# Optimization experiments

Measured on AMD Instinct MI355X. Metric: run time of the kernel, lower is better.

Reference implementation:

```python
import jax, jax.numpy as jnp
import numpy as np

B, S, D, H = 2, 2048, 512, 8
DK = D // H
NEG = -1.0e9


def _xavier(key, shape):
    fan_in, fan_out = shape[-1], shape[0]
    lim = np.sqrt(6.0 / (fan_in + fan_out))
    return jax.random.uniform(key, shape, jnp.float32, -lim, lim)


def _rope_freqs(seq, dim):
    # lucidrains RotaryEmbedding: inv_freq over even dims, each freq repeated twice
    inv_freq = 1.0 / (10000.0 ** (jnp.arange(0, dim, 2, dtype=jnp.float32) / dim))
    freqs = jnp.arange(seq, dtype=jnp.float32)[:, None] * inv_freq[None, :]  # (S, dim/2)
    return jnp.repeat(freqs, 2, axis=-1)  # (S, dim)


def _rotate_half(x):
    xr = x.reshape(*x.shape[:-1], -1, 2)
    x1, x2 = xr[..., 0], xr[..., 1]
    return jnp.stack([-x2, x1], axis=-1).reshape(x.shape)


def _shift_down(s):
    # pad_zero row at position 0, drop last-but-keep rows 1: (concat trick)
    return jnp.concatenate([jnp.zeros_like(s[:, :, :1, :]), s[:, :, 1:, :]], axis=2)


def setup_inputs() -> dict:
    key = jax.random.key(0)
    kq, kk, kv, kt, kwq, kwk, kwv, kwo, kg = jax.random.split(key, 9)
    inp = {
        "q": jax.random.normal(kq, (B, S, D), jnp.float32),
        "k": jax.random.normal(kk, (B, S, D), jnp.float32),
        "v": jax.random.normal(kv, (B, S, D), jnp.float32),
        "ltime": jax.random.uniform(kt, (B, S), jnp.float32),
        "mask": jnp.broadcast_to(jnp.triu(jnp.ones((S, S), bool), k=1)[None], (B, S, S)),
        "Wq": _xavier(kwq, (D, D)), "bq": jnp.zeros((D,), jnp.float32),
        "Wk": _xavier(kwk, (D, D)), "bk": jnp.zeros((D,), jnp.float32),
        "Wv": _xavier(kwv, (D, D)), "bv": jnp.zeros((D,), jnp.float32),
        "Wo": _xavier(kwo, (D, D)), "bo": jnp.zeros((D,), jnp.float32),
        "gammas": jax.random.uniform(kg, (H, S, 1), jnp.float32, -0.1, 0.1),
    }
    return inp


def reference(q, k, v, ltime, mask, Wq, bq, Wk, bk, Wv, bv, Wo, bo, gammas):
    del ltime  # used only in dead code (dist_seq) in the original module

    def proj(x, W, b):
        return (x @ W.T + b).reshape(B, S, H, DK).transpose(0, 2, 1, 3)  # (B,H,S,DK)

    qh, kh, vh = proj(q, Wq, bq), proj(k, Wk, bk), proj(v, Wv, bv)

    freqs = _rope_freqs(S, DK)[None, None]  # (1,1,S,DK)
    cos, sin = jnp.cos(freqs), jnp.sin(freqs)
    qh = qh * cos + _rotate_half(qh) * sin
    kh = kh * cos + _rotate_half(kh) * sin

    scores = jnp.einsum("bhid,bhjd->bhij", qh, kh) / np.sqrt(DK)
    m = mask[:, None]  # (B,1,S,S)

    # --- no_grad distance-decay block ---
    s_ = jax.nn.softmax(jnp.where(m, NEG, scores), axis=-1)
    s_ = _shift_down(s_)
    distcum = jnp.cumsum(s_, axis=-1)
    disttot = jnp.sum(s_, axis=-1, keepdims=True)
    idx = jnp.arange(S, dtype=jnp.float32)
    pos_eff = jnp.abs(idx[None, :] - idx[:, None])[None, None]  # (1,1,S,S)
    dist = jax.lax.stop_gradient(
        jnp.sqrt(jnp.maximum((disttot - distcum) * pos_eff, 0.0)))

    g = -jax.nn.softplus(gammas)[None]  # (1,H,S,1)
    total_effect = jnp.clip(jnp.exp(dist * g), 1e-5, 1e5)
    scores = total_effect * scores

    scores = jax.nn.softmax(jnp.where(m, NEG, scores), axis=-1)
    scores = _shift_down(scores)

    out = jnp.einsum("bhij,bhjd->bhid", scores, vh)  # (B,H,S,DK)
    out = out.transpose(0, 2, 1, 3).reshape(B, S, D)
    return out @ Wo.T + bo
```

## Files before the change

### kernel.cpp

```cpp
#include <hip/hip_runtime.h>
#include <math.h>

#define B_ 2
#define S_ 2048
#define D_ 512
#define H_ 8
#define DK_ 64

typedef __attribute__((ext_vector_type(8))) short bf16x8;
typedef __attribute__((ext_vector_type(4))) float f32x4;

#define MFMA16(A, Bv, C) __builtin_amdgcn_mfma_f32_16x16x32_bf16(A, Bv, C, 0, 0, 0)

__device__ inline unsigned short f2bf(float x) {
  unsigned u = __float_as_uint(x);
  unsigned r = (u + 0x7fffu + ((u >> 16) & 1u)) >> 16;
  return (unsigned short)r;
}
__device__ inline unsigned pack2(float a, float b) {
  return (unsigned)f2bf(a) | ((unsigned)f2bf(b) << 16);
}

__global__ void rope_table_k(float* cs) {
  int idx = blockIdx.x * blockDim.x + threadIdx.x;
  if (idx >= S_ * 32) return;
  int s = idx >> 5, i = idx & 31;
  float invf = powf(10000.0f, -(float)(2 * i) / 64.0f);
  float ang = (float)s * invf;
  double a = (double)ang;
  cs[idx * 2]     = (float)cos(a);
  cs[idx * 2 + 1] = (float)sin(a);
}

__global__ __launch_bounds__(256)
void cvt3_k(const float* __restrict__ a, const float* __restrict__ b,
            const float* __restrict__ c, unsigned short* __restrict__ dst) {
  size_t idx = ((size_t)blockIdx.x * 256 + threadIdx.x) * 4;
  const size_t per = (size_t)4096 * 512;
  const float* src; size_t r;
  if (idx < per)            { src = a; r = idx; }
  else if (idx < 2 * per)   { src = b; r = idx - per; }
  else                      { src = c; r = idx - 2 * per; }
  float4 x = *(const float4*)(src + r);
  ushort4 y = { f2bf(x.x), f2bf(x.y), f2bf(x.z), f2bf(x.w) };
  *(ushort4*)(dst + idx) = y;
}
__global__ __launch_bounds__(256)
void cvt4_k(const float* __restrict__ a, const float* __restrict__ b,
            const float* __restrict__ c, const float* __restrict__ d,
            unsigned short* __restrict__ dst) {
  size_t idx = ((size_t)blockIdx.x * 256 + threadIdx.x) * 4;
  const size_t per = (size_t)512 * 512;
  const float* src; size_t r;
  if (idx < per)            { src = a; r = idx; }
  else if (idx < 2 * per)   { src = b; r = idx - per; }
  else if (idx < 3 * per)   { src = c; r = idx - 2 * per; }
  else                      { src = d; r = idx - 3 * per; }
  float4 x = *(const float4*)(src + r);
  ushort4 y = { f2bf(x.x), f2bf(x.y), f2bf(x.z), f2bf(x.w) };
  *(ushort4*)(dst + idx) = y;
}

__global__ __launch_bounds__(256)
void gemm_bf(const unsigned short* __restrict__ A,
             const unsigned short* __restrict__ W,
             const float* __restrict__ bias, void* __restrict__ Cout,
             const float* __restrict__ cs, int mode) {
  const int bm = blockIdx.y * 64, bn = blockIdx.x * 64;
  const int tid = threadIdx.x, w = tid >> 6, lane = tid & 63;
  const int li = lane & 15, lg = lane >> 4;
  __shared__ __align__(16) unsigned short As[64 * 64];
  __shared__ __align__(16) unsigned short Ws[64 * 64];
  f32x4 acc[4] = {{0.f,0.f,0.f,0.f},{0.f,0.f,0.f,0.f},{0.f,0.f,0.f,0.f},{0.f,0.f,0.f,0.f}};

  const int Bo0 = tid * 16, Bo1 = tid * 16 + 4096;
  const int r0 = Bo0 >> 7, c0 = Bo0 & 127;
  const int r1 = Bo1 >> 7, c1 = Bo1 & 127;
  const int so0 = (r0 * 128 + (c0 ^ ((r0 & 7) << 4))) >> 1;
  const int so1 = (r1 * 128 + (c1 ^ ((r1 & 7) << 4))) >> 1;

  const char* Abase = (const char*)A;
  const char* Wbase = (const char*)W;
  uint4 ra0 = *(const uint4*)(Abase + (size_t)(bm + r0) * 1024 + c0);
  uint4 ra1 = *(const uint4*)(Abase + (size_t)(bm + r1) * 1024 + c1);
  uint4 rw0 = *(const uint4*)(Wbase + (size_t)(bn + r0) * 1024 + c0);
  uint4 rw1 = *(const uint4*)(Wbase + (size_t)(bn + r1) * 1024 + c1);

  for (int t = 0; t < 8; ++t) {
    __syncthreads();
    *(uint4*)&As[so0] = ra0; *(uint4*)&As[so1] = ra1;
    *(uint4*)&Ws[so0] = rw0; *(uint4*)&Ws[so1] = rw1;
    __syncthreads();
    if (t < 7) {
      int k0 = (t + 1) * 128;
      ra0 = *(const uint4*)(Abase + (size_t)(bm + r0) * 1024 + k0 + c0);
      ra1 = *(const uint4*)(Abase + (size_t)(bm + r1) * 1024 + k0 + c1);
      rw0 = *(const uint4*)(Wbase + (size_t)(bn + r0) * 1024 + k0 + c0);
      rw1 = *(const uint4*)(Wbase + (size_t)(bn + r1) * 1024 + k0 + c1);
    }
#pragma unroll
    for (int kk = 0; kk < 2; ++kk) {
      const int brow = w * 16 + li;
      bf16x8 bf = *(const bf16x8*)&Ws[brow * 64 + (((kk * 64 + lg * 16) ^ ((brow & 7) << 4)) >> 1)];
#pragma unroll
      for (int mt = 0; mt < 4; ++mt) {
        const int arow = mt * 16 + li;
        bf16x8 af = *(const bf16x8*)&As[arow * 64 + (((kk * 64 + lg * 16) ^ ((arow & 7) << 4)) >> 1)];
        acc[mt] = MFMA16(af, bf, acc[mt]);
      }
    }
  }

  const int n = bn + w * 16 + li;
  const float bv = bias[n];
  if (mode == 0) {
    float* C = (float*)Cout;
#pragma unroll
    for (int mt = 0; mt < 4; ++mt)
#pragma unroll
      for (int r = 0; r < 4; ++r) {
        int m = bm + mt * 16 + lg * 4 + r;
        C[(size_t)m * 512 + n] = acc[mt][r] + bv;
      }
  } else if (mode == 1) {
    unsigned short* C = (unsigned short*)Cout;
    const int d = n & 63, hh = n >> 6, p = d >> 1;
#pragma unroll
    for (int mt = 0; mt < 4; ++mt)
#pragma unroll
      for (int r = 0; r < 4; ++r) {
        int m = bm + mt * 16 + lg * 4 + r;
        int bb = m >> 11, sp = m & (S_ - 1);
        float val = acc[mt][r] + bv;
        float other = __shfl_xor(val, 1, 64);
        const float* cp = cs + ((size_t)sp * 32 + p) * 2;
        float cc = cp[0], sn = cp[1];
        float y = (d & 1) ? (val * cc + other * sn) : (val * cc - other * sn);
        C[(((size_t)bb * H_ + hh) * S_ + sp) * DK_ + d] = f2bf(y);
      }
  } else {
    unsigned short* C = (unsigned short*)Cout;
    const int d = n & 63, hh = n >> 6;
#pragma unroll
    for (int mt = 0; mt < 4; ++mt) {
      int m0 = bm + mt * 16 + lg * 4;
      int bb = m0 >> 11, sp0 = m0 & (S_ - 1);
      ushort4 y = { f2bf(acc[mt][0] + bv), f2bf(acc[mt][1] + bv),
                    f2bf(acc[mt][2] + bv), f2bf(acc[mt][3] + bv) };
      *(ushort4*)&C[(((size_t)bb * H_ + hh) * DK_ + d) * S_ + sp0] = y;
    }
  }
}

__global__ __launch_bounds__(256)
void attn3(const unsigned short* __restrict__ Qbf,
           const unsigned short* __restrict__ Kbf,
           const unsigned short* __restrict__ Vtbf,
           const float* __restrict__ gammas,
           unsigned short* __restrict__ out_pre) {
  const int qt = 127 - (int)blockIdx.x;
  const int bh = blockIdx.y;
  const int h = bh & (H_ - 1), b = bh >> 3;
  const int i0 = qt * 16;
  const int tid = threadIdx.x;
  const int w = tid >> 6, lane = tid & 63;
  const int li = lane & 15, lg = lane >> 4;
  const int i = i0 + li;

  __shared__ __align__(16) unsigned short P[4][16][40];
  __shared__ float sm1[4][16], sden[4][16], sm2[4][16], sl2[4][16];
  __shared__ float Obuf[4][64][17];

  const unsigned short* Qp = Qbf + (size_t)bh * (S_ * DK_);
  const unsigned short* Kp = Kbf + (size_t)bh * (S_ * DK_);
  const unsigned short* Vp = Vtbf + (size_t)bh * (DK_ * S_);

  bf16x8 qb0 = *(const bf16x8*)(Qp + (size_t)i * DK_ + lg * 8);
  bf16x8 qb1 = *(const bf16x8*)(Qp + (size_t)i * DK_ + 32 + lg * 8);

  const int ntile = (i0 >> 5) + 1;
  const int nt4 = (ntile + 3) >> 2;
  const int tb = (w * nt4 < ntile) ? w * nt4 : ntile;
  const int te = (tb + nt4 < ntile) ? tb + nt4 : ntile;

  const float g = -log1pf(__expf(gammas[h * S_ + i]));

  float m1w = -INFINITY, denw = 0.f;
  bf16x8 ka0, ka1, ka2, ka3;
  if (tb < te) {
    const int jb = tb * 32;
    const unsigned short* p0 = Kp + (size_t)(jb + li) * DK_ + lg * 8;
    const unsigned short* p1 = Kp + (size_t)(jb + 16 + li) * DK_ + lg * 8;
    ka0 = *(const bf16x8*)p0; ka1 = *(const bf16x8*)(p0 + 32);
    ka2 = *(const bf16x8*)p1; ka3 = *(const bf16x8*)(p1 + 32);
  }
  for (int t = tb; t < te; ++t) {
    const int j0 = t * 32;
    const bool pf = (t + 1 < te);
    bf16x8 na0, na1, na2, na3;
    if (pf) {
      const unsigned short* p0 = Kp + (size_t)(j0 + 32 + li) * DK_ + lg * 8;
      const unsigned short* p1 = Kp + (size_t)(j0 + 48 + li) * DK_ + lg * 8;
      na0 = *(const bf16x8*)p0; na1 = *(const bf16x8*)(p0 + 32);
      na2 = *(const bf16x8*)p1; na3 = *(const bf16x8*)(p1 + 32);
    }
    f32x4 acc0 = {0.f,0.f,0.f,0.f}, acc1 = {0.f,0.f,0.f,0.f};
    acc0 = MFMA16(ka0, qb0, acc0); acc0 = MFMA16(ka1, qb1, acc0);
    acc1 = MFMA16(ka2, qb0, acc1); acc1 = MFMA16(ka3, qb1, acc1);
    float sv[8]; float mloc = -INFINITY;
#pragma unroll
    for (int x = 0; x < 8; ++x) {
      float s = ((x < 4) ? acc0[x & 3] : acc1[x & 3]) * 0.125f;
      sv[x] = s;
      int j = j0 + ((x >> 2) << 4) + lg * 4 + (x & 3);
      mloc = fmaxf(mloc, (j <= i) ? s : -INFINITY);
    }
    mloc = fmaxf(mloc, __shfl_xor(mloc, 16, 64));
    mloc = fmaxf(mloc, __shfl_xor(mloc, 32, 64));
    float mn = fmaxf(m1w, mloc);
    float sc = __expf(m1w - mn);
    float ls = 0.f;
#pragma unroll
    for (int x = 0; x < 8; ++x) {
      int j = j0 + ((x >> 2) << 4) + lg * 4 + (x & 3);
      ls += (j <= i) ? __expf(sv[x] - mn) : 0.f;
    }
    ls += __shfl_xor(ls, 16, 64);
    ls += __shfl_xor(ls, 32, 64);
    denw = denw * sc + ls;
    m1w = mn;
    if (pf) { ka0 = na0; ka1 = na1; ka2 = na2; ka3 = na3; }
  }
  if (lg == 0) { sm1[w][li] = m1w; sden[w][li] = denw; }
  __syncthreads();

  const float gm0 = sm1[0][li], gm1v = sm1[1][li], gm2v = sm1[2][li], gm3v = sm1[3][li];
  const float m1 = fmaxf(fmaxf(gm0, gm1v), fmaxf(gm2v, gm3v));
  const float d0 = sden[0][li] * __expf(gm0 - m1);
  const float d1 = sden[1][li] * __expf(gm1v - m1);
  const float d2 = sden[2][li] * __expf(gm2v - m1);
  const float d3 = sden[3][li] * __expf(gm3v - m1);
  const float den = d0 + d1 + d2 + d3;
  const float inv1 = 1.f / den;
  float cum = 0.f;
  if (w > 0) cum += d0;
  if (w > 1) cum += d1;
  if (w > 2) cum += d2;

  float m2w = -INFINITY, l2w = 0.f;
  f32x4 o0 = {0.f,0.f,0.f,0.f}, o1 = {0.f,0.f,0.f,0.f};
  f32x4 o2 = {0.f,0.f,0.f,0.f}, o3 = {0.f,0.f,0.f,0.f};
  bf16x8 va0, va1, va2, va3;
  if (tb < te) {
    const int jb = tb * 32;
    const unsigned short* p0 = Kp + (size_t)(jb + li) * DK_ + lg * 8;
    const unsigned short* p1 = Kp + (size_t)(jb + 16 + li) * DK_ + lg * 8;
    ka0 = *(const bf16x8*)p0; ka1 = *(const bf16x8*)(p0 + 32);
    ka2 = *(const bf16x8*)p1; ka3 = *(const bf16x8*)(p1 + 32);
    va0 = *(const bf16x8*)(Vp + (size_t)li * S_ + jb + lg * 8);
    va1 = *(const bf16x8*)(Vp + (size_t)(16 + li) * S_ + jb + lg * 8);
    va2 = *(const bf16x8*)(Vp + (size_t)(32 + li) * S_ + jb + lg * 8);
    va3 = *(const bf16x8*)(Vp + (size_t)(48 + li) * S_ + jb + lg * 8);
  }
  for (int t = tb; t < te; ++t) {
    const int j0 = t * 32;
    const bool pf = (t + 1 < te);
    bf16x8 na0, na1, na2, na3, nv0, nv1, nv2, nv3;
    if (pf) {
      const int j1 = j0 + 32;
      const unsigned short* p0 = Kp + (size_t)(j1 + li) * DK_ + lg * 8;
      const unsigned short* p1 = Kp + (size_t)(j1 + 16 + li) * DK_ + lg * 8;
      na0 = *(const bf16x8*)p0; na1 = *(const bf16x8*)(p0 + 32);
      na2 = *(const bf16x8*)p1; na3 = *(const bf16x8*)(p1 + 32);
      nv0 = *(const bf16x8*)(Vp + (size_t)li * S_ + j1 + lg * 8);
      nv1 = *(const bf16x8*)(Vp + (size_t)(16 + li) * S_ + j1 + lg * 8);
      nv2 = *(const bf16x8*)(Vp + (size_t)(32 + li) * S_ + j1 + lg * 8);
      nv3 = *(const bf16x8*)(Vp + (size_t)(48 + li) * S_ + j1 + lg * 8);
    }
    f32x4 acc0 = {0.f,0.f,0.f,0.f}, acc1 = {0.f,0.f,0.f,0.f};
    acc0 = MFMA16(ka0, qb0, acc0); acc0 = MFMA16(ka1, qb1, acc0);
    acc1 = MFMA16(ka2, qb0, acc1); acc1 = MFMA16(ka3, qb1, acc1);

    float sv[8], ev[8]; bool uv[8];
#pragma unroll
    for (int x = 0; x < 8; ++x) {
      float s = ((x < 4) ? acc0[x & 3] : acc1[x & 3]) * 0.125f;
      sv[x] = s;
      int j = j0 + ((x >> 2) << 4) + lg * 4 + (x & 3);
      uv[x] = (j <= i);
      ev[x] = uv[x] ? __expf(s - m1) : 0.f;
    }
    float L0 = ev[0] + ev[1] + ev[2] + ev[3];
    float L1 = ev[4] + ev[5] + ev[6] + ev[7];
    float v0 = L0;
    { float tt = __shfl_up(v0, 16, 64); if (lg >= 1) v0 += tt;
      tt = __shfl_up(v0, 32, 64); if (lg >= 2) v0 += tt; }
    float tot0 = __shfl(v0, li + 48, 64);
    float v1 = L1;
    { float tt = __shfl_up(v1, 16, 64); if (lg >= 1) v1 += tt;
      tt = __shfl_up(v1, 32, 64); if (lg >= 2) v1 += tt; }
    float tot1 = __shfl(v1, li + 48, 64);
    float base0 = cum + (v0 - L0);
    float base1 = cum + tot0 + (v1 - L1);
    cum += tot0 + tot1;

    float s2[8]; float run = base0;
#pragma unroll
    for (int x = 0; x < 8; ++x) {
      if (x == 4) run = base1;
      run += ev[x];
      int j = j0 + ((x >> 2) << 4) + lg * 4 + (x & 3);
      float rem = fmaxf(1.f - run * inv1, 0.f);
      float dist = sqrtf(fmaxf(rem * (float)(i - j), 0.f));
      float te2 = fminf(fmaxf(__expf(dist * g), 1e-5f), 1e5f);
      s2[x] = uv[x] ? te2 * sv[x] : -INFINITY;
    }
    float mloc = s2[0];
#pragma unroll
    for (int x = 1; x < 8; ++x) mloc = fmaxf(mloc, s2[x]);
    mloc = fmaxf(mloc, __shfl_xor(mloc, 16, 64));
    mloc = fmaxf(mloc, __shfl_xor(mloc, 32, 64));
    float mn = fmaxf(m2w, mloc);
    float f = __expf(m2w - mn);
    float p[8]; float ls = 0.f;
#pragma unroll
    for (int x = 0; x < 8; ++x) { p[x] = __expf(s2[x] - mn); ls += p[x]; }
    ls += __shfl_xor(ls, 16, 64);
    ls += __shfl_xor(ls, 32, 64);
    l2w = l2w * f + ls;
    m2w = mn;
    o0 *= f; o1 *= f; o2 *= f; o3 *= f;

    { uint2 w0v = { pack2(p[0], p[1]), pack2(p[2], p[3]) };
      uint2 w1v = { pack2(p[4], p[5]), pack2(p[6], p[7]) };
      *(uint2*)&P[w][li][lg * 4] = w0v;
      *(uint2*)&P[w][li][16 + lg * 4] = w1v; }
    bf16x8 pb = *(const bf16x8*)&P[w][li][lg * 8];
    o0 = MFMA16(va0, pb, o0);
    o1 = MFMA16(va1, pb, o1);
    o2 = MFMA16(va2, pb, o2);
    o3 = MFMA16(va3, pb, o3);

    if (pf) { ka0 = na0; ka1 = na1; ka2 = na2; ka3 = na3;
              va0 = nv0; va1 = nv1; va2 = nv2; va3 = nv3; }
  }

  if (lg == 0) { sm2[w][li] = m2w; sl2[w][li] = l2w; }
  {
    f32x4 oo[4] = { o0, o1, o2, o3 };
#pragma unroll
    for (int db = 0; db < 4; ++db)
#pragma unroll
      for (int e = 0; e < 4; ++e)
        Obuf[w][lane][db * 4 + e] = oo[db][e];
  }
  __syncthreads();
  if (w == 0) {
    const float q0 = sm2[0][li], q1 = sm2[1][li], q2 = sm2[2][li], q3 = sm2[3][li];
    const float m2 = fmaxf(fmaxf(q0, q1), fmaxf(q2, q3));
    const float f0 = __expf(q0 - m2), f1 = __expf(q1 - m2);
    const float f2 = __expf(q2 - m2), f3 = __expf(q3 - m2);
    const float l2 = sl2[0][li] * f0 + sl2[1][li] * f1 + sl2[2][li] * f2 + sl2[3][li] * f3;
    const float z = (i == 0) ? 0.f : (1.f / l2);
    unsigned short* dst = out_pre + ((size_t)(b * S_ + i)) * D_ + h * DK_;
#pragma unroll
    for (int db = 0; db < 4; ++db) {
      float vo[4];
#pragma unroll
      for (int e = 0; e < 4; ++e)
        vo[e] = (Obuf[0][lane][db * 4 + e] * f0 + Obuf[1][lane][db * 4 + e] * f1 +
                 Obuf[2][lane][db * 4 + e] * f2 + Obuf[3][lane][db * 4 + e] * f3) * z;
      ushort4 y = { f2bf(vo[0]), f2bf(vo[1]), f2bf(vo[2]), f2bf(vo[3]) };
      *(ushort4*)&dst[db * 16 + lg * 4] = y;
    }
  }
}

extern "C" void kernel_launch(void* const* d_in, const int* in_sizes, int n_in,
                              void* d_out, int out_size, void* d_ws, size_t ws_size,
                              hipStream_t stream) {
  const float* q  = (const float*)d_in[0];
  const float* k  = (const float*)d_in[1];
  const float* v  = (const float*)d_in[2];
  const float* Wq = (const float*)d_in[5];
  const float* bq = (const float*)d_in[6];
  const float* Wk = (const float*)d_in[7];
  const float* bk = (const float*)d_in[8];
  const float* Wv = (const float*)d_in[9];
  const float* bv = (const float*)d_in[10];
  const float* Wo = (const float*)d_in[11];
  const float* bo = (const float*)d_in[12];
  const float* gammas = (const float*)d_in[13];
  float* out = (float*)d_out;

  float* cs = (float*)d_ws;
  unsigned short* Abf  = (unsigned short*)(cs + (size_t)S_ * 32 * 2);
  unsigned short* Wbf  = Abf + (size_t)3 * 4096 * 512;
  unsigned short* Qbf  = Wbf + (size_t)4 * 512 * 512;
  unsigned short* Kbf  = Qbf + (size_t)B_ * H_ * S_ * DK_;
  unsigned short* Vtbf = Kbf + (size_t)B_ * H_ * S_ * DK_;
  unsigned short* out_pre = Vtbf + (size_t)B_ * H_ * S_ * DK_;

  rope_table_k<<<(S_ * 32 + 255) / 256, 256, 0, stream>>>(cs);
  cvt3_k<<<6144, 256, 0, stream>>>(q, k, v, Abf);
  cvt4_k<<<1024, 256, 0, stream>>>(Wq, Wk, Wv, Wo, Wbf);

  const size_t nA = (size_t)4096 * 512;
  const size_t nW = (size_t)512 * 512;
  dim3 gg(8, 64);
  gemm_bf<<<gg, 256, 0, stream>>>(Abf,          Wbf,          bq, Qbf,  cs, 1);
  gemm_bf<<<gg, 256, 0, stream>>>(Abf + nA,     Wbf + nW,     bk, Kbf,  cs, 1);
  gemm_bf<<<gg, 256, 0, stream>>>(Abf + 2 * nA, Wbf + 2 * nW, bv, Vtbf, cs, 2);

  attn3<<<dim3(128, B_ * H_), 256, 0, stream>>>(Qbf, Kbf, Vtbf, gammas, out_pre);

  gemm_bf<<<gg, 256, 0, stream>>>(out_pre, Wbf + 3 * nW, bo, out, cs, 0);
}
```

Before: 285.5 us.

## Use async LDS-staged 128x64 GEMM tiles and pair causal query tiles in attention

The GEMM kernel becomes a 128x64 tile with a 2x2 warp layout. It double-buffers LDS filled through global_load_lds direct-to-LDS loads with an XOR-swizzled layout, which replaces the register-staged copy and the second barrier per step. The attention kernel now has each block process two query tiles, a long one (127-bx) and a short one (bx), so causal work is balanced across 64 blocks per head instead of 128 uneven ones. The cost is fewer blocks, which lowers occupancy and parallelism, and more LDS per GEMM block.

```diff
diff --git a/kernel.cpp b/kernel.cpp
--- a/kernel.cpp
+++ b/kernel.cpp
@@ -19,6 +19,10 @@
 }
 __device__ inline unsigned pack2(float a, float b) {
   return (unsigned)f2bf(a) | ((unsigned)f2bf(b) << 16);
+}
+__device__ __forceinline__ void gload16(const void* g, void* l) {
+  __builtin_amdgcn_global_load_lds((const __attribute__((address_space(1))) unsigned*)g,
+                                   (__attribute__((address_space(3))) unsigned*)l, 16, 0, 0);
 }
 
 __global__ void rope_table_k(float* cs) {
@@ -62,92 +66,107 @@
 }
 
 __global__ __launch_bounds__(256)
-void gemm_bf(const unsigned short* __restrict__ A,
-             const unsigned short* __restrict__ W,
-             const float* __restrict__ bias, void* __restrict__ Cout,
-             const float* __restrict__ cs, int mode) {
-  const int bm = blockIdx.y * 64, bn = blockIdx.x * 64;
+void gemm2(const unsigned short* __restrict__ A,
+           const unsigned short* __restrict__ W,
+           const float* __restrict__ bias, void* __restrict__ Cout,
+           const float* __restrict__ cs, int mode) {
+  const int bm = blockIdx.y * 128, bn = blockIdx.x * 64;
   const int tid = threadIdx.x, w = tid >> 6, lane = tid & 63;
   const int li = lane & 15, lg = lane >> 4;
-  __shared__ __align__(16) unsigned short As[64 * 64];
-  __shared__ __align__(16) unsigned short Ws[64 * 64];
-  f32x4 acc[4] = {{0.f,0.f,0.f,0.f},{0.f,0.f,0.f,0.f},{0.f,0.f,0.f,0.f},{0.f,0.f,0.f,0.f}};
-
-  const int Bo0 = tid * 16, Bo1 = tid * 16 + 4096;
-  const int r0 = Bo0 >> 7, c0 = Bo0 & 127;
-  const int r1 = Bo1 >> 7, c1 = Bo1 & 127;
-  const int so0 = (r0 * 128 + (c0 ^ ((r0 & 7) << 4))) >> 1;
-  const int so1 = (r1 * 128 + (c1 ^ ((r1 & 7) << 4))) >> 1;
+  const int wr = w >> 1, wc = w & 1;
+
+  __shared__ __align__(16) unsigned short As[2][128 * 64];
+  __shared__ __align__(16) unsigned short Ws[2][64 * 64];
+
+  f32x4 acc[4][2] = {};
 
   const char* Abase = (const char*)A;
   const char* Wbase = (const char*)W;
-  uint4 ra0 = *(const uint4*)(Abase + (size_t)(bm + r0) * 1024 + c0);
-  uint4 ra1 = *(const uint4*)(Abase + (size_t)(bm + r1) * 1024 + c1);
-  uint4 rw0 = *(const uint4*)(Wbase + (size_t)(bn + r0) * 1024 + c0);
-  uint4 rw1 = *(const uint4*)(Wbase + (size_t)(bn + r1) * 1024 + c1);
-
+  const int lr = lane >> 3;
+  const int lc = (lane & 7) ^ lr;
+
+  auto stage = [&](int buf, int t) {
+    const char* Ab = Abase + (size_t)bm * 1024 + t * 128;
+    const char* Wb = Wbase + (size_t)bn * 1024 + t * 128;
+    char* AsB = (char*)&As[buf][0];
+    char* WsB = (char*)&Ws[buf][0];
+#pragma unroll
+    for (int it = 0; it < 4; ++it) {
+      int R0 = (w * 4 + it) * 8;
+      gload16(Ab + (size_t)(R0 + lr) * 1024 + lc * 16, AsB + R0 * 128);
+    }
+#pragma unroll
+    for (int it = 0; it < 2; ++it) {
+      int R0 = (w * 2 + it) * 8;
+      gload16(Wb + (size_t)(R0 + lr) * 1024 + lc * 16, WsB + R0 * 128);
+    }
+  };
+
+  stage(0, 0);
+  int cur = 0;
   for (int t = 0; t < 8; ++t) {
     __syncthreads();
-    *(uint4*)&As[so0] = ra0; *(uint4*)&As[so1] = ra1;
-    *(uint4*)&Ws[so0] = rw0; *(uint4*)&Ws[so1] = rw1;
-    __syncthreads();
-    if (t < 7) {
-      int k0 = (t + 1) * 128;
-      ra0 = *(const uint4*)(Abase + (size_t)(bm + r0) * 1024 + k0 + c0);
-      ra1 = *(const uint4*)(Abase + (size_t)(bm + r1) * 1024 + k0 + c1);
-      rw0 = *(const uint4*)(Wbase + (size_t)(bn + r0) * 1024 + k0 + c0);
-      rw1 = *(const uint4*)(Wbase + (size_t)(bn + r1) * 1024 + k0 + c1);
-    }
+    if (t < 7) stage(cur ^ 1, t + 1);
 #pragma unroll
     for (int kk = 0; kk < 2; ++kk) {
-      const int brow = w * 16 + li;
-      bf16x8 bf = *(const bf16x8*)&Ws[brow * 64 + (((kk * 64 + lg * 16) ^ ((brow & 7) << 4)) >> 1)];
+      const int chunk = lg + kk * 4;
+      bf16x8 bfr[2];
+#pragma unroll
+      for (int nt = 0; nt < 2; ++nt) {
+        int row = wc * 32 + nt * 16 + li;
+        bfr[nt] = *(const bf16x8*)&Ws[cur][row * 64 + ((chunk ^ (row & 7)) << 3)];
+      }
 #pragma unroll
       for (int mt = 0; mt < 4; ++mt) {
-        const int arow = mt * 16 + li;
-        bf16x8 af = *(const bf16x8*)&As[arow * 64 + (((kk * 64 + lg * 16) ^ ((arow & 7) << 4)) >> 1)];
-        acc[mt] = MFMA16(af, bf, acc[mt]);
-      }
-    }
+        int row = wr * 64 + mt * 16 + li;
+        bf16x8 af = *(const bf16x8*)&As[cur][row * 64 + ((chunk ^ (row & 7)) << 3)];
+        acc[mt][0] = MFMA16(af, bfr[0], acc[mt][0]);
+        acc[mt][1] = MFMA16(af, bfr[1], acc[mt][1]);
+      }
+    }
+    cur ^= 1;
   }
 
-  const int n = bn + w * 16 + li;
-  const float bv = bias[n];
-  if (mode == 0) {
-    float* C = (float*)Cout;
-#pragma unroll
-    for (int mt = 0; mt < 4; ++mt)
-#pragma unroll
-      for (int r = 0; r < 4; ++r) {
-        int m = bm + mt * 16 + lg * 4 + r;
-        C[(size_t)m * 512 + n] = acc[mt][r] + bv;
-      }
-  } else if (mode == 1) {
-    unsigned short* C = (unsigned short*)Cout;
-    const int d = n & 63, hh = n >> 6, p = d >> 1;
-#pragma unroll
-    for (int mt = 0; mt < 4; ++mt)
-#pragma unroll
-      for (int r = 0; r < 4; ++r) {
-        int m = bm + mt * 16 + lg * 4 + r;
-        int bb = m >> 11, sp = m & (S_ - 1);
-        float val = acc[mt][r] + bv;
-        float other = __shfl_xor(val, 1, 64);
-        const float* cp = cs + ((size_t)sp * 32 + p) * 2;
-        float cc = cp[0], sn = cp[1];
-        float y = (d & 1) ? (val * cc + other * sn) : (val * cc - other * sn);
-        C[(((size_t)bb * H_ + hh) * S_ + sp) * DK_ + d] = f2bf(y);
-      }
-  } else {
-    unsigned short* C = (unsigned short*)Cout;
-    const int d = n & 63, hh = n >> 6;
-#pragma unroll
-    for (int mt = 0; mt < 4; ++mt) {
-      int m0 = bm + mt * 16 + lg * 4;
-      int bb = m0 >> 11, sp0 = m0 & (S_ - 1);
-      ushort4 y = { f2bf(acc[mt][0] + bv), f2bf(acc[mt][1] + bv),
-                    f2bf(acc[mt][2] + bv), f2bf(acc[mt][3] + bv) };
-      *(ushort4*)&C[(((size_t)bb * H_ + hh) * DK_ + d) * S_ + sp0] = y;
+#pragma unroll
+  for (int nt = 0; nt < 2; ++nt) {
+    const int n = bn + wc * 32 + nt * 16 + li;
+    const float bv = bias[n];
+    if (mode == 0) {
+      float* C = (float*)Cout;
+#pragma unroll
+      for (int mt = 0; mt < 4; ++mt)
+#pragma unroll
+        for (int r = 0; r < 4; ++r) {
+          int m = bm + wr * 64 + mt * 16 + lg * 4 + r;
+          C[(size_t)m * 512 + n] = acc[mt][nt][r] + bv;
+        }
+    } else if (mode == 1) {
+      unsigned short* C = (unsigned short*)Cout;
+      const int d = n & 63, hh = n >> 6, p = d >> 1;
+#pragma unroll
+      for (int mt = 0; mt < 4; ++mt)
+#pragma unroll
+        for (int r = 0; r < 4; ++r) {
+          int m = bm + wr * 64 + mt * 16 + lg * 4 + r;
+          int bb = m >> 11, sp = m & (S_ - 1);
+          float val = acc[mt][nt][r] + bv;
+          float other = __shfl_xor(val, 1, 64);
+          const float* cp = cs + ((size_t)sp * 32 + p) * 2;
+          float cc = cp[0], sn = cp[1];
+          float y = (d & 1) ? (val * cc + other * sn) : (val * cc - other * sn);
+          C[(((size_t)bb * H_ + hh) * S_ + sp) * DK_ + d] = f2bf(y);
+        }
+    } else {
+      unsigned short* C = (unsigned short*)Cout;
+      const int d = n & 63, hh = n >> 6;
+#pragma unroll
+      for (int mt = 0; mt < 4; ++mt) {
+        int m0 = bm + wr * 64 + mt * 16 + lg * 4;
+        int bb = m0 >> 11, sp0 = m0 & (S_ - 1);
+        ushort4 y = { f2bf(acc[mt][nt][0] + bv), f2bf(acc[mt][nt][1] + bv),
+                      f2bf(acc[mt][nt][2] + bv), f2bf(acc[mt][nt][3] + bv) };
+        *(ushort4*)&C[(((size_t)bb * H_ + hh) * DK_ + d) * S_ + sp0] = y;
+      }
     }
   }
 }
@@ -158,14 +177,12 @@
            const unsigned short* __restrict__ Vtbf,
            const float* __restrict__ gammas,
            unsigned short* __restrict__ out_pre) {
-  const int qt = 127 - (int)blockIdx.x;
+  const int bx = (int)blockIdx.x;
   const int bh = blockIdx.y;
   const int h = bh & (H_ - 1), b = bh >> 3;
-  const int i0 = qt * 16;
   const int tid = threadIdx.x;
   const int w = tid >> 6, lane = tid & 63;
   const int li = lane & 15, lg = lane >> 4;
-  const int i = i0 + li;
 
   __shared__ __align__(16) unsigned short P[4][16][40];
   __shared__ float sm1[4][16], sden[4][16], sm2[4][16], sl2[4][16];
@@ -175,203 +192,209 @@
   const unsigned short* Kp = Kbf + (size_t)bh * (S_ * DK_);
   const unsigned short* Vp = Vtbf + (size_t)bh * (DK_ * S_);
 
-  bf16x8 qb0 = *(const bf16x8*)(Qp + (size_t)i * DK_ + lg * 8);
-  bf16x8 qb1 = *(const bf16x8*)(Qp + (size_t)i * DK_ + 32 + lg * 8);
-
-  const int ntile = (i0 >> 5) + 1;
-  const int nt4 = (ntile + 3) >> 2;
-  const int tb = (w * nt4 < ntile) ? w * nt4 : ntile;
-  const int te = (tb + nt4 < ntile) ? tb + nt4 : ntile;
-
-  const float g = -log1pf(__expf(gammas[h * S_ + i]));
-
-  float m1w = -INFINITY, denw = 0.f;
-  bf16x8 ka0, ka1, ka2, ka3;
-  if (tb < te) {
-    const int jb = tb * 32;
-    const unsigned short* p0 = Kp + (size_t)(jb + li) * DK_ + lg * 8;
-    const unsigned short* p1 = Kp + (size_t)(jb + 16 + li) * DK_ + lg * 8;
-    ka0 = *(const bf16x8*)p0; ka1 = *(const bf16x8*)(p0 + 32);
-    ka2 = *(const bf16x8*)p1; ka3 = *(const bf16x8*)(p1 + 32);
-  }
-  for (int t = tb; t < te; ++t) {
-    const int j0 = t * 32;
-    const bool pf = (t + 1 < te);
-    bf16x8 na0, na1, na2, na3;
-    if (pf) {
-      const unsigned short* p0 = Kp + (size_t)(j0 + 32 + li) * DK_ + lg * 8;
-      const unsigned short* p1 = Kp + (size_t)(j0 + 48 + li) * DK_ + lg * 8;
-      na0 = *(const bf16x8*)p0; na1 = *(const bf16x8*)(p0 + 32);
-      na2 = *(const bf16x8*)p1; na3 = *(const bf16x8*)(p1 + 32);
-    }
-    f32x4 acc0 = {0.f,0.f,0.f,0.f}, acc1 = {0.f,0.f,0.f,0.f};
-    acc0 = MFMA16(ka0, qb0, acc0); acc0 = MFMA16(ka1, qb1, acc0);
-    acc1 = MFMA16(ka2, qb0, acc1); acc1 = MFMA16(ka3, qb1, acc1);
-    float sv[8]; float mloc = -INFINITY;
-#pragma unroll
-    for (int x = 0; x < 8; ++x) {
-      float s = ((x < 4) ? acc0[x & 3] : acc1[x & 3]) * 0.125f;
-      sv[x] = s;
-      int j = j0 + ((x >> 2) << 4) + lg * 4 + (x & 3);
-      mloc = fmaxf(mloc, (j <= i) ? s : -INFINITY);
-    }
-    mloc = fmaxf(mloc, __shfl_xor(mloc, 16, 64));
-    mloc = fmaxf(mloc, __shfl_xor(mloc, 32, 64));
-    float mn = fmaxf(m1w, mloc);
-    float sc = __expf(m1w - mn);
-    float ls = 0.f;
-#pragma unroll
-    for (int x = 0; x < 8; ++x) {
-      int j = j0 + ((x >> 2) << 4) + lg * 4 + (x & 3);
-      ls += (j <= i) ? __expf(sv[x] - mn) : 0.f;
-    }
-    ls += __shfl_xor(ls, 16, 64);
-    ls += __shfl_xor(ls, 32, 64);
-    denw = denw * sc + ls;
-    m1w = mn;
-    if (pf) { ka0 = na0; ka1 = na1; ka2 = na2; ka3 = na3; }
-  }
-  if (lg == 0) { sm1[w][li] = m1w; sden[w][li] = denw; }
-  __syncthreads();
-
-  const float gm0 = sm1[0][li], gm1v = sm1[1][li], gm2v = sm1[2][li], gm3v = sm1[3][li];
-  const float m1 = fmaxf(fmaxf(gm0, gm1v), fmaxf(gm2v, gm3v));
-  const float d0 = sden[0][li] * __expf(gm0 - m1);
-  const float d1 = sden[1][li] * __expf(gm1v - m1);
-  const float d2 = sden[2][li] * __expf(gm2v - m1);
-  const float d3 = sden[3][li] * __expf(gm3v - m1);
-  const float den = d0 + d1 + d2 + d3;
-  const float inv1 = 1.f / den;
-  float cum = 0.f;
-  if (w > 0) cum += d0;
-  if (w > 1) cum += d1;
-  if (w > 2) cum += d2;
-
-  float m2w = -INFINITY, l2w = 0.f;
-  f32x4 o0 = {0.f,0.f,0.f,0.f}, o1 = {0.f,0.f,0.f,0.f};
-  f32x4 o2 = {0.f,0.f,0.f,0.f}, o3 = {0.f,0.f,0.f,0.f};
-  bf16x8 va0, va1, va2, va3;
-  if (tb < te) {
-    const int jb = tb * 32;
-    const unsigned short* p0 = Kp + (size_t)(jb + li) * DK_ + lg * 8;
-    const unsigned short* p1 = Kp + (size_t)(jb + 16 + li) * DK_ + lg * 8;
-    ka0 = *(const bf16x8*)p0; ka1 = *(const bf16x8*)(p0 + 32);
-    ka2 = *(const bf16x8*)p1; ka3 = *(const bf16x8*)(p1 + 32);
-    va0 = *(const bf16x8*)(Vp + (size_t)li * S_ + jb + lg * 8);
-    va1 = *(const bf16x8*)(Vp + (size_t)(16 + li) * S_ + jb + lg * 8);
-    va2 = *(const bf16x8*)(Vp + (size_t)(32 + li) * S_ + jb + lg * 8);
-    va3 = *(const bf16x8*)(Vp + (size_t)(48 + li) * S_ + jb + lg * 8);
-  }
-  for (int t = tb; t < te; ++t) {
-    const int j0 = t * 32;
-    const bool pf = (t + 1 < te);
-    bf16x8 na0, na1, na2, na3, nv0, nv1, nv2, nv3;
-    if (pf) {
-      const int j1 = j0 + 32;
-      const unsigned short* p0 = Kp + (size_t)(j1 + li) * DK_ + lg * 8;
-      const unsigned short* p1 = Kp + (size_t)(j1 + 16 + li) * DK_ + lg * 8;
-      na0 = *(const bf16x8*)p0; na1 = *(const bf16x8*)(p0 + 32);
-      na2 = *(const bf16x8*)p1; na3 = *(const bf16x8*)(p1 + 32);
-      nv0 = *(const bf16x8*)(Vp + (size_t)li * S_ + j1 + lg * 8);
-      nv1 = *(const bf16x8*)(Vp + (size_t)(16 + li) * S_ + j1 + lg * 8);
-      nv2 = *(const bf16x8*)(Vp + (size_t)(32 + li) * S_ + j1 + lg * 8);
-      nv3 = *(const bf16x8*)(Vp + (size_t)(48 + li) * S_ + j1 + lg * 8);
-    }
-    f32x4 acc0 = {0.f,0.f,0.f,0.f}, acc1 = {0.f,0.f,0.f,0.f};
-    acc0 = MFMA16(ka0, qb0, acc0); acc0 = MFMA16(ka1, qb1, acc0);
-    acc1 = MFMA16(ka2, qb0, acc1); acc1 = MFMA16(ka3, qb1, acc1);
-
-    float sv[8], ev[8]; bool uv[8];
-#pragma unroll
-    for (int x = 0; x < 8; ++x) {
-      float s = ((x < 4) ? acc0[x & 3] : acc1[x & 3]) * 0.125f;
-      sv[x] = s;
-      int j = j0 + ((x >> 2) << 4) + lg * 4 + (x & 3);
-      uv[x] = (j <= i);
-      ev[x] = uv[x] ? __expf(s - m1) : 0.f;
-    }
-    float L0 = ev[0] + ev[1] + ev[2] + ev[3];
-    float L1 = ev[4] + ev[5] + ev[6] + ev[7];
-    float v0 = L0;
-    { float tt = __shfl_up(v0, 16, 64); if (lg >= 1) v0 += tt;
-      tt = __shfl_up(v0, 32, 64); if (lg >= 2) v0 += tt; }
-    float tot0 = __shfl(v0, li + 48, 64);
-    float v1 = L1;
-    { float tt = __shfl_up(v1, 16, 64); if (lg >= 1) v1 += tt;
-      tt = __shfl_up(v1, 32, 64); if (lg >= 2) v1 += tt; }
-    float tot1 = __shfl(v1, li + 48, 64);
-    float base0 = cum + (v0 - L0);
-    float base1 = cum + tot0 + (v1 - L1);
-    cum += tot0 + tot1;
-
-    float s2[8]; float run = base0;
-#pragma unroll
-    for (int x = 0; x < 8; ++x) {
-      if (x == 4) run = base1;
-      run += ev[x];
-      int j = j0 + ((x >> 2) << 4) + lg * 4 + (x & 3);
-      float rem = fmaxf(1.f - run * inv1, 0.f);
-      float dist = sqrtf(fmaxf(rem * (float)(i - j), 0.f));
-      float te2 = fminf(fmaxf(__expf(dist * g), 1e-5f), 1e5f);
-      s2[x] = uv[x] ? te2 * sv[x] : -INFINITY;
-    }
-    float mloc = s2[0];
-#pragma unroll
-    for (int x = 1; x < 8; ++x) mloc = fmaxf(mloc, s2[x]);
-    mloc = fmaxf(mloc, __shfl_xor(mloc, 16, 64));
-    mloc = fmaxf(mloc, __shfl_xor(mloc, 32, 64));
-    float mn = fmaxf(m2w, mloc);
-    float f = __expf(m2w - mn);
-    float p[8]; float ls = 0.f;
-#pragma unroll
-    for (int x = 0; x < 8; ++x) { p[x] = __expf(s2[x] - mn); ls += p[x]; }
-    ls += __shfl_xor(ls, 16, 64);
-    ls += __shfl_xor(ls, 32, 64);
-    l2w = l2w * f + ls;
-    m2w = mn;
-    o0 *= f; o1 *= f; o2 *= f; o3 *= f;
-
-    { uint2 w0v = { pack2(p[0], p[1]), pack2(p[2], p[3]) };
-      uint2 w1v = { pack2(p[4], p[5]), pack2(p[6], p[7]) };
-      *(uint2*)&P[w][li][lg * 4] = w0v;
-      *(uint2*)&P[w][li][16 + lg * 4] = w1v; }
-    bf16x8 pb = *(const bf16x8*)&P[w][li][lg * 8];
-    o0 = MFMA16(va0, pb, o0);
-    o1 = MFMA16(va1, pb, o1);
-    o2 = MFMA16(va2, pb, o2);
-    o3 = MFMA16(va3, pb, o3);
-
-    if (pf) { ka0 = na0; ka1 = na1; ka2 = na2; ka3 = na3;
-              va0 = nv0; va1 = nv1; va2 = nv2; va3 = nv3; }
-  }
-
-  if (lg == 0) { sm2[w][li] = m2w; sl2[w][li] = l2w; }
-  {
-    f32x4 oo[4] = { o0, o1, o2, o3 };
-#pragma unroll
-    for (int db = 0; db < 4; ++db)
-#pragma unroll
-      for (int e = 0; e < 4; ++e)
-        Obuf[w][lane][db * 4 + e] = oo[db][e];
-  }
-  __syncthreads();
-  if (w == 0) {
-    const float q0 = sm2[0][li], q1 = sm2[1][li], q2 = sm2[2][li], q3 = sm2[3][li];
-    const float m2 = fmaxf(fmaxf(q0, q1), fmaxf(q2, q3));
-    const float f0 = __expf(q0 - m2), f1 = __expf(q1 - m2);
-    const float f2 = __expf(q2 - m2), f3 = __expf(q3 - m2);
-    const float l2 = sl2[0][li] * f0 + sl2[1][li] * f1 + sl2[2][li] * f2 + sl2[3][li] * f3;
-    const float z = (i == 0) ? 0.f : (1.f / l2);
-    unsigned short* dst = out_pre + ((size_t)(b * S_ + i)) * D_ + h * DK_;
-#pragma unroll
-    for (int db = 0; db < 4; ++db) {
-      float vo[4];
-#pragma unroll
-      for (int e = 0; e < 4; ++e)
-        vo[e] = (Obuf[0][lane][db * 4 + e] * f0 + Obuf[1][lane][db * 4 + e] * f1 +
-                 Obuf[2][lane][db * 4 + e] * f2 + Obuf[3][lane][db * 4 + e] * f3) * z;
-      ushort4 y = { f2bf(vo[0]), f2bf(vo[1]), f2bf(vo[2]), f2bf(vo[3]) };
-      *(ushort4*)&dst[db * 16 + lg * 4] = y;
+  for (int half = 0; half < 2; ++half) {
+    const int qt = half ? bx : (127 - bx);
+    const int i0 = qt * 16;
+    const int i = i0 + li;
+
+    bf16x8 qb0 = *(const bf16x8*)(Qp + (size_t)i * DK_ + lg * 8);
+    bf16x8 qb1 = *(const bf16x8*)(Qp + (size_t)i * DK_ + 32 + lg * 8);
+
+    const int ntile = (i0 >> 5) + 1;
+    const int nt4 = (ntile + 3) >> 2;
+    const int tb = (w * nt4 < ntile) ? w * nt4 : ntile;
+    const int te = (tb + nt4 < ntile) ? tb + nt4 : ntile;
+
+    const float g = -log1pf(__expf(gammas[h * S_ + i]));
+
+    float m1w = -INFINITY, denw = 0.f;
+    bf16x8 ka0, ka1, ka2, ka3;
+    if (tb < te) {
+      const int jb = tb * 32;
+      const unsigned short* p0 = Kp + (size_t)(jb + li) * DK_ + lg * 8;
+      const unsigned short* p1 = Kp + (size_t)(jb + 16 + li) * DK_ + lg * 8;
+      ka0 = *(const bf16x8*)p0; ka1 = *(const bf16x8*)(p0 + 32);
+      ka2 = *(const bf16x8*)p1; ka3 = *(const bf16x8*)(p1 + 32);
+    }
+    for (int t = tb; t < te; ++t) {
+      const int j0 = t * 32;
+      const bool pf = (t + 1 < te);
+      bf16x8 na0, na1, na2, na3;
+      if (pf) {
+        const unsigned short* p0 = Kp + (size_t)(j0 + 32 + li) * DK_ + lg * 8;
+        const unsigned short* p1 = Kp + (size_t)(j0 + 48 + li) * DK_ + lg * 8;
+        na0 = *(const bf16x8*)p0; na1 = *(const bf16x8*)(p0 + 32);
+        na2 = *(const bf16x8*)p1; na3 = *(const bf16x8*)(p1 + 32);
+      }
+      f32x4 acc0 = {0.f,0.f,0.f,0.f}, acc1 = {0.f,0.f,0.f,0.f};
+      acc0 = MFMA16(ka0, qb0, acc0); acc0 = MFMA16(ka1, qb1, acc0);
+      acc1 = MFMA16(ka2, qb0, acc1); acc1 = MFMA16(ka3, qb1, acc1);
+      float sv[8]; float mloc = -INFINITY;
+#pragma unroll
+      for (int x = 0; x < 8; ++x) {
+        float s = ((x < 4) ? acc0[x & 3] : acc1[x & 3]) * 0.125f;
+        sv[x] = s;
+        int j = j0 + ((x >> 2) << 4) + lg * 4 + (x & 3);
+        mloc = fmaxf(mloc, (j <= i) ? s : -INFINITY);
+      }
+      mloc = fmaxf(mloc, __shfl_xor(mloc, 16, 64));
+      mloc = fmaxf(mloc, __shfl_xor(mloc, 32, 64));
+      float mn = fmaxf(m1w, mloc);
+      float sc = __expf(m1w - mn);
+      float ls = 0.f;
+#pragma unroll
+      for (int x = 0; x < 8; ++x) {
+        int j = j0 + ((x >> 2) << 4) + lg * 4 + (x & 3);
+        ls += (j <= i) ? __expf(sv[x] - mn) : 0.f;
+      }
+      ls += __shfl_xor(ls, 16, 64);
+      ls += __shfl_xor(ls, 32, 64);
+      denw = denw * sc + ls;
+      m1w = mn;
+      if (pf) { ka0 = na0; ka1 = na1; ka2 = na2; ka3 = na3; }
+    }
+    if (lg == 0) { sm1[w][li] = m1w; sden[w][li] = denw; }
+    __syncthreads();
+
+    const float gm0 = sm1[0][li], gm1v = sm1[1][li], gm2v = sm1[2][li], gm3v = sm1[3][li];
+    const float m1 = fmaxf(fmaxf(gm0, gm1v), fmaxf(gm2v, gm3v));
+    const float d0 = sden[0][li] * __expf(gm0 - m1);
+    const float d1 = sden[1][li] * __expf(gm1v - m1);
+    const float d2 = sden[2][li] * __expf(gm2v - m1);
+    const float d3 = sden[3][li] * __expf(gm3v - m1);
+    const float den = d0 + d1 + d2 + d3;
+    const float inv1 = 1.f / den;
+    float cum = 0.f;
+    if (w > 0) cum += d0;
+    if (w > 1) cum += d1;
+    if (w > 2) cum += d2;
+
+    float m2w = -INFINITY, l2w = 0.f;
+    f32x4 o0 = {0.f,0.f,0.f,0.f}, o1 = {0.f,0.f,0.f,0.f};
+    f32x4 o2 = {0.f,0.f,0.f,0.f}, o3 = {0.f,0.f,0.f,0.f};
+    bf16x8 va0, va1, va2, va3;
+    if (tb < te) {
+      const int jb = tb * 32;
+      const unsigned short* p0 = Kp + (size_t)(jb + li) * DK_ + lg * 8;
+      const unsigned short* p1 = Kp + (size_t)(jb + 16 + li) * DK_ + lg * 8;
+      ka0 = *(const bf16x8*)p0; ka1 = *(const bf16x8*)(p0 + 32);
+      ka2 = *(const bf16x8*)p1; ka3 = *(const bf16x8*)(p1 + 32);
+      va0 = *(const bf16x8*)(Vp + (size_t)li * S_ + jb + lg * 8);
+      va1 = *(const bf16x8*)(Vp + (size_t)(16 + li) * S_ + jb + lg * 8);
+      va2 = *(const bf16x8*)(Vp + (size_t)(32 + li) * S_ + jb + lg * 8);
+      va3 = *(const bf16x8*)(Vp + (size_t)(48 + li) * S_ + jb + lg * 8);
+    }
+    for (int t = tb; t < te; ++t) {
+      const int j0 = t * 32;
+      const bool pf = (t + 1 < te);
+      bf16x8 na0, na1, na2, na3, nv0, nv1, nv2, nv3;
+      if (pf) {
+        const int j1 = j0 + 32;
+        const unsigned short* p0 = Kp + (size_t)(j1 + li) * DK_ + lg * 8;
+        const unsigned short* p1 = Kp + (size_t)(j1 + 16 + li) * DK_ + lg * 8;
+        na0 = *(const bf16x8*)p0; na1 = *(const bf16x8*)(p0 + 32);
+        na2 = *(const bf16x8*)p1; na3 = *(const bf16x8*)(p1 + 32);
+        nv0 = *(const bf16x8*)(Vp + (size_t)li * S_ + j1 + lg * 8);
+        nv1 = *(const bf16x8*)(Vp + (size_t)(16 + li) * S_ + j1 + lg * 8);
+        nv2 = *(const bf16x8*)(Vp + (size_t)(32 + li) * S_ + j1 + lg * 8);
+        nv3 = *(const bf16x8*)(Vp + (size_t)(48 + li) * S_ + j1 + lg * 8);
+      }
+      f32x4 acc0 = {0.f,0.f,0.f,0.f}, acc1 = {0.f,0.f,0.f,0.f};
+      acc0 = MFMA16(ka0, qb0, acc0); acc0 = MFMA16(ka1, qb1, acc0);
+      acc1 = MFMA16(ka2, qb0, acc1); acc1 = MFMA16(ka3, qb1, acc1);
+
+      float sv[8], ev[8]; bool uv[8];
+#pragma unroll
+      for (int x = 0; x < 8; ++x) {
+        float s = ((x < 4) ? acc0[x & 3] : acc1[x & 3]) * 0.125f;
+        sv[x] = s;
+        int j = j0 + ((x >> 2) << 4) + lg * 4 + (x & 3);
+        uv[x] = (j <= i);
+        ev[x] = uv[x] ? __expf(s - m1) : 0.f;
+      }
+      float L0 = ev[0] + ev[1] + ev[2] + ev[3];
+      float L1 = ev[4] + ev[5] + ev[6] + ev[7];
+      float v0 = L0;
+      { float tt = __shfl_up(v0, 16, 64); if (lg >= 1) v0 += tt;
+        tt = __shfl_up(v0, 32, 64); if (lg >= 2) v0 += tt; }
+      float tot0 = __shfl(v0, li + 48, 64);
+      float v1 = L1;
+      { float tt = __shfl_up(v1, 16, 64); if (lg >= 1) v1 += tt;
+        tt = __shfl_up(v1, 32, 64); if (lg >= 2) v1 += tt; }
+      float tot1 = __shfl(v1, li + 48, 64);
+      float base0 = cum + (v0 - L0);
+      float base1 = cum + tot0 + (v1 - L1);
+      cum += tot0 + tot1;
+
+      float s2[8]; float run = base0;
+#pragma unroll
+      for (int x = 0; x < 8; ++x) {
+        if (x == 4) run = base1;
+        run += ev[x];
+        int j = j0 + ((x >> 2) << 4) + lg * 4 + (x & 3);
+        float rem = fmaxf(1.f - run * inv1, 0.f);
+        float dist = sqrtf(fmaxf(rem * (float)(i - j), 0.f));
+        float te2 = fminf(fmaxf(__expf(dist * g), 1e-5f), 1e5f);
+        s2[x] = uv[x] ? te2 * sv[x] : -INFINITY;
+      }
+      float mloc = s2[0];
+#pragma unroll
+      for (int x = 1; x < 8; ++x) mloc = fmaxf(mloc, s2[x]);
+      mloc = fmaxf(mloc, __shfl_xor(mloc, 16, 64));
+      mloc = fmaxf(mloc, __shfl_xor(mloc, 32, 64));
+      float mn = fmaxf(m2w, mloc);
+      float f = __expf(m2w - mn);
+      float p[8]; float ls = 0.f;
+#pragma unroll
+      for (int x = 0; x < 8; ++x) { p[x] = __expf(s2[x] - mn); ls += p[x]; }
+      ls += __shfl_xor(ls, 16, 64);
+      ls += __shfl_xor(ls, 32, 64);
+      l2w = l2w * f + ls;
+      m2w = mn;
+      o0 *= f; o1 *= f; o2 *= f; o3 *= f;
+
+      { uint2 w0v = { pack2(p[0], p[1]), pack2(p[2], p[3]) };
+        uint2 w1v = { pack2(p[4], p[5]), pack2(p[6], p[7]) };
+        *(uint2*)&P[w][li][lg * 4] = w0v;
+        *(uint2*)&P[w][li][16 + lg * 4] = w1v; }
+      bf16x8 pb = *(const bf16x8*)&P[w][li][lg * 8];
+      o0 = MFMA16(va0, pb, o0);
+      o1 = MFMA16(va1, pb, o1);
+      o2 = MFMA16(va2, pb, o2);
+      o3 = MFMA16(va3, pb, o3);
+
+      if (pf) { ka0 = na0; ka1 = na1; ka2 = na2; ka3 = na3;
+                va0 = nv0; va1 = nv1; va2 = nv2; va3 = nv3; }
+    }
+
+    if (lg == 0) { sm2[w][li] = m2w; sl2[w][li] = l2w; }
+    {
+      f32x4 oo[4] = { o0, o1, o2, o3 };
+#pragma unroll
+      for (int db = 0; db < 4; ++db)
+#pragma unroll
+        for (int e = 0; e < 4; ++e)
+          Obuf[w][lane][db * 4 + e] = oo[db][e];
+    }
+    __syncthreads();
+    if (w == 0) {
+      const float q0 = sm2[0][li], q1 = sm2[1][li], q2 = sm2[2][li], q3 = sm2[3][li];
+      const float m2 = fmaxf(fmaxf(q0, q1), fmaxf(q2, q3));
+      const float f0 = __expf(q0 - m2), f1 = __expf(q1 - m2);
+      const float f2 = __expf(q2 - m2), f3 = __expf(q3 - m2);
+      const float l2 = sl2[0][li] * f0 + sl2[1][li] * f1 + sl2[2][li] * f2 + sl2[3][li] * f3;
+      const float z = (i == 0) ? 0.f : (1.f / l2);
+      unsigned short* dst = out_pre + ((size_t)(b * S_ + i)) * D_ + h * DK_;
+#pragma unroll
+      for (int db = 0; db < 4; ++db) {
+        float vo[4];
+#pragma unroll
+        for (int e = 0; e < 4; ++e)
+          vo[e] = (Obuf[0][lane][db * 4 + e] * f0 + Obuf[1][lane][db * 4 + e] * f1 +
+                   Obuf[2][lane][db * 4 + e] * f2 + Obuf[3][lane][db * 4 + e] * f3) * z;
+        ushort4 y = { f2bf(vo[0]), f2bf(vo[1]), f2bf(vo[2]), f2bf(vo[3]) };
+        *(ushort4*)&dst[db * 16 + lg * 4] = y;
+      }
     }
   }
 }
@@ -407,12 +430,12 @@
 
   const size_t nA = (size_t)4096 * 512;
   const size_t nW = (size_t)512 * 512;
-  dim3 gg(8, 64);
-  gemm_bf<<<gg, 256, 0, stream>>>(Abf,          Wbf,          bq, Qbf,  cs, 1);
-  gemm_bf<<<gg, 256, 0, stream>>>(Abf + nA,     Wbf + nW,     bk, Kbf,  cs, 1);
-  gemm_bf<<<gg, 256, 0, stream>>>(Abf + 2 * nA, Wbf + 2 * nW, bv, Vtbf, cs, 2);
-
-  attn3<<<dim3(128, B_ * H_), 256, 0, stream>>>(Qbf, Kbf, Vtbf, gammas, out_pre);
-
-  gemm_bf<<<gg, 256, 0, stream>>>(out_pre, Wbf + 3 * nW, bo, out, cs, 0);
-}
+  dim3 gg(8, 32);
+  gemm2<<<gg, 256, 0, stream>>>(Abf,          Wbf,          bq, Qbf,  cs, 1);
+  gemm2<<<gg, 256, 0, stream>>>(Abf + nA,     Wbf + nW,     bk, Kbf,  cs, 1);
+  gemm2<<<gg, 256, 0, stream>>>(Abf + 2 * nA, Wbf + 2 * nW, bv, Vtbf, cs, 2);
+
+  attn3<<<dim3(64, B_ * H_), 256, 0, stream>>>(Qbf, Kbf, Vtbf, gammas, out_pre);
+
+  gemm2<<<gg, 256, 0, stream>>>(out_pre, Wbf + 3 * nW, bo, out, cs, 0);
+}
```

New measurement: 270.8 us. 1.05x faster.
